# Kernel optimization log

Measured on AMD Instinct MI355X. Metric: run time of the kernel, lower is better.

## Reference

```python
import jax, jax.numpy as jnp
import numpy as np

N_NODES = 10000
N_EDGES = 160000
IN_CH = 512
HID = 512


def setup_inputs() -> dict:
    key = jax.random.key(0)
    k1, k2, k3, k4, k5, k6 = jax.random.split(key, 6)
    x = jax.random.normal(k1, (N_NODES, IN_CH), dtype=jnp.float32)
    # Linear weight, xavier-uniform style scale (torch stores [out, in])
    lim = float(np.sqrt(6.0 / (IN_CH + HID)))
    fc_w = jax.random.uniform(k2, (HID, IN_CH), dtype=jnp.float32, minval=-lim, maxval=lim)
    bias = jnp.zeros((HID,), dtype=jnp.float32)
    prelu_a = jnp.full((1,), 0.25, dtype=jnp.float32)  # torch PReLU default slope
    adj_vals = jax.random.uniform(k3, (N_EDGES,), dtype=jnp.float32)
    adj_row = jnp.sort(jax.random.randint(k4, (N_EDGES,), 0, N_NODES, dtype=jnp.int64))
    adj_col = jax.random.randint(k5, (N_EDGES,), 0, N_NODES, dtype=jnp.int64)
    return {"x": x, "fc_w": fc_w, "bias": bias, "prelu_a": prelu_a,
            "adj_vals": adj_vals, "adj_row": adj_row, "adj_col": adj_col}


def reference(x, fc_w, bias, prelu_a, adj_vals, adj_row, adj_col):
    n_nodes = x.shape[0]
    # x_fts = self.fc(x)  (no bias in fc)
    x_fts = x @ fc_w.T                                   # [N, HID]
    # out = torch.spmm(adj, x_fts): sparse COO matmul via gather + segment_sum
    gathered = adj_vals[:, None] * x_fts[adj_col]        # [E, HID]
    out = jax.ops.segment_sum(gathered, adj_row, num_segments=n_nodes)
    out = out + bias                                     # [N, HID]
    # PReLU with single learned slope
    return jnp.where(out >= 0, out, prelu_a * out)
```

## Files before the change

kernel.cpp:

```cpp
#include <hip/hip_runtime.h>
#include <hip/hip_bf16.h>

typedef __attribute__((ext_vector_type(4))) float f32x4;
typedef __attribute__((ext_vector_type(8))) short bf16x8;

#define NNODES 10000
#define KDIM 512
#define NDIM 512
#define NEDGES 160000
#define RP_BLOCKS 40
#define QV_BLOCKS 157
#define SIDE_BLOCKS (RP_BLOCKS + QV_BLOCKS)
#define GEMM_BLOCKS 628

#define XSCALE 6.0f
#define XQ (127.0f / XSCALE)
#define OUTK (XSCALE / (127.0f * 127.0f))

__device__ __forceinline__ unsigned short f2bf(float f) {
    __hip_bfloat16 h = __float2bfloat16(f);
    return *reinterpret_cast<unsigned short*>(&h);
}

__device__ __forceinline__ bf16x8 cvt8(float4 a, float4 b) {
    bf16x8 r;
    r[0] = (short)f2bf(a.x); r[1] = (short)f2bf(a.y);
    r[2] = (short)f2bf(a.z); r[3] = (short)f2bf(a.w);
    r[4] = (short)f2bf(b.x); r[5] = (short)f2bf(b.y);
    r[6] = (short)f2bf(b.z); r[7] = (short)f2bf(b.w);
    return r;
}

__device__ __forceinline__ int q127(float v, float s) {
    return (int)rintf(fminf(fmaxf(v * s, -127.f), 127.f));
}

#if __has_builtin(__builtin_amdgcn_sdot4)
#define DOT4(a, b, c) __builtin_amdgcn_sdot4((a), (b), (c), false)
#else
__device__ __forceinline__ int dot4_sw(int a, int b, int c) {
    c += (int)(signed char)(a) * (int)(signed char)(b);
    c += (int)(signed char)(a >> 8) * (int)(signed char)(b >> 8);
    c += (int)(signed char)(a >> 16) * (int)(signed char)(b >> 16);
    c += (a >> 24) * (b >> 24);
    return c;
}
#define DOT4(a, b, c) dot4_sw((a), (b), (c))
#endif

__global__ __launch_bounds__(256) void gemm_prep_kernel(
    const float* __restrict__ A, const float* __restrict__ B,
    signed char* __restrict__ X8,
    const int* __restrict__ rows, int* __restrict__ row_ptr,
    const float* __restrict__ vals, int* __restrict__ qvals, int M) {
    __shared__ unsigned short lA[2][64 * 64];
    __shared__ unsigned short lB[2][128 * 64];

    if (blockIdx.x < RP_BLOCKS) {
        int i = blockIdx.x * 256 + threadIdx.x;
        if (i <= NNODES) {
            int lo = 0, hi = NEDGES;
            while (lo < hi) { int mid = (lo + hi) >> 1; if (rows[mid] < i) lo = mid + 1; else hi = mid; }
            row_ptr[i] = lo;
        }
        return;
    }
    if (blockIdx.x < SIDE_BLOCKS) {
        int i = (blockIdx.x - RP_BLOCKS) * 1024 + threadIdx.x * 4;
        if (i < NEDGES) {
            float4 v = *reinterpret_cast<const float4*>(vals + i);
            int4 o;
            o.x = q127(v.x, 127.f); o.y = q127(v.y, 127.f);
            o.z = q127(v.z, 127.f); o.w = q127(v.w, 127.f);
            *reinterpret_cast<int4*>(qvals + i) = o;
        }
        return;
    }

    const int orig = blockIdx.x - SIDE_BLOCKS;
    const int xcd = orig & 7;
    const int base = (xcd < 4) ? xcd * 79 : 4 * 79 + (xcd - 4) * 78;
    const int wgid = base + (orig >> 3);

    const int tid = threadIdx.x;
    const int wid = tid >> 6;
    const int lane = tid & 63;
    const int wc = wid;
    const int m0 = (wgid >> 2) * 64;
    const int n0 = (wgid & 3) * 128;

    const int ar0 = tid >> 3, ar1 = (tid + 256) >> 3;
    const int ag = tid & 7;
    int agr0 = m0 + ar0; if (agr0 >= M) agr0 = M - 1;
    int agr1 = m0 + ar1; if (agr1 >= M) agr1 = M - 1;
    const float* pa0 = A + (size_t)agr0 * KDIM + ag * 8;
    const float* pa1 = A + (size_t)agr1 * KDIM + ag * 8;
    const int wA0 = ar0 * 64 + (ag ^ (ar0 & 7)) * 8;
    const int wA1 = ar1 * 64 + (ag ^ (ar1 & 7)) * 8;
    const int br = tid >> 3;
    const float* pb0 = B + (size_t)(n0 + br) * KDIM + ag * 8;
    const float* pb1 = B + (size_t)(n0 + br + 32) * KDIM + ag * 8;
    const float* pb2 = B + (size_t)(n0 + br + 64) * KDIM + ag * 8;
    const float* pb3 = B + (size_t)(n0 + br + 96) * KDIM + ag * 8;
    const int wB = br * 64 + (ag ^ (br & 7)) * 8;

    f32x4 acc[4][2] = {};
    float4 la0, la1, la2, la3, lb0, lb1, lb2, lb3, lb4, lb5, lb6, lb7;

#define GLOAD(k0)                                                \
    la0 = *reinterpret_cast<const float4*>(pa0 + (k0));          \
    la1 = *reinterpret_cast<const float4*>(pa0 + (k0) + 4);      \
    la2 = *reinterpret_cast<const float4*>(pa1 + (k0));          \
    la3 = *reinterpret_cast<const float4*>(pa1 + (k0) + 4);      \
    lb0 = *reinterpret_cast<const float4*>(pb0 + (k0));          \
    lb1 = *reinterpret_cast<const float4*>(pb0 + (k0) + 4);      \
    lb2 = *reinterpret_cast<const float4*>(pb1 + (k0));          \
    lb3 = *reinterpret_cast<const float4*>(pb1 + (k0) + 4);      \
    lb4 = *reinterpret_cast<const float4*>(pb2 + (k0));          \
    lb5 = *reinterpret_cast<const float4*>(pb2 + (k0) + 4);      \
    lb6 = *reinterpret_cast<const float4*>(pb3 + (k0));          \
    lb7 = *reinterpret_cast<const float4*>(pb3 + (k0) + 4);

#define LWRITE(buf)                                                          \
    *reinterpret_cast<bf16x8*>(lA[buf] + wA0) = cvt8(la0, la1);              \
    *reinterpret_cast<bf16x8*>(lA[buf] + wA1) = cvt8(la2, la3);              \
    *reinterpret_cast<bf16x8*>(lB[buf] + wB) = cvt8(lb0, lb1);               \
    *reinterpret_cast<bf16x8*>(lB[buf] + wB + 32 * 64) = cvt8(lb2, lb3);     \
    *reinterpret_cast<bf16x8*>(lB[buf] + wB + 64 * 64) = cvt8(lb4, lb5);     \
    *reinterpret_cast<bf16x8*>(lB[buf] + wB + 96 * 64) = cvt8(lb6, lb7);

    GLOAD(0)
    LWRITE(0)
    __syncthreads();
    int cur = 0;
#pragma unroll
    for (int kt = 0; kt < 8; kt++) {
        if (kt + 1 < 8) { GLOAD((kt + 1) * 64) }

        bf16x8 af[4][2], bfr[2][2];
#pragma unroll
        for (int i = 0; i < 4; i++)
#pragma unroll
            for (int h = 0; h < 2; h++) {
                int row = i * 16 + (lane & 15);
                int s = (lane >> 4) + h * 4;
                af[i][h] = *reinterpret_cast<const bf16x8*>(
                    lA[cur] + (size_t)row * 64 + (size_t)(s ^ (row & 7)) * 8);
            }
#pragma unroll
        for (int j = 0; j < 2; j++)
#pragma unroll
            for (int h = 0; h < 2; h++) {
                int row = wc * 32 + j * 16 + (lane & 15);
                int s = (lane >> 4) + h * 4;
                bfr[j][h] = *reinterpret_cast<const bf16x8*>(
                    lB[cur] + (size_t)row * 64 + (size_t)(s ^ (row & 7)) * 8);
            }
#pragma unroll
        for (int h = 0; h < 2; h++)
#pragma unroll
            for (int i = 0; i < 4; i++)
#pragma unroll
                for (int j = 0; j < 2; j++)
                    acc[i][j] = __builtin_amdgcn_mfma_f32_16x16x32_bf16(af[i][h], bfr[j][h], acc[i][j], 0, 0, 0);

        if (kt + 1 < 8) { LWRITE(cur ^ 1) }
        __syncthreads();
        cur ^= 1;
    }

#pragma unroll
    for (int i = 0; i < 4; i++) {
#pragma unroll
        for (int r = 0; r < 4; r++) {
            int row = m0 + i * 16 + (lane >> 4) * 4 + r;
            if (row < M) {
#pragma unroll
                for (int j = 0; j < 2; j++) {
                    int col = n0 + wc * 32 + j * 16 + (lane & 15);
                    X8[(size_t)row * NDIM + col] = (signed char)q127(acc[i][j][r], XQ);
                }
            }
        }
    }
}

#define BT4(T0, T1, T2, T3, w0, w1, w2, w3)                          \
    {                                                                \
        unsigned ab_lo = __builtin_amdgcn_perm(w1, w0, 0x05010400u); \
        unsigned ab_hi = __builtin_amdgcn_perm(w1, w0, 0x07030602u); \
        unsigned cd_lo = __builtin_amdgcn_perm(w3, w2, 0x05010400u); \
        unsigned cd_hi = __builtin_amdgcn_perm(w3, w2, 0x07030602u); \
        T0 = __builtin_amdgcn_perm(cd_lo, ab_lo, 0x05040100u);       \
        T1 = __builtin_amdgcn_perm(cd_lo, ab_lo, 0x07060302u);       \
        T2 = __builtin_amdgcn_perm(cd_hi, ab_hi, 0x05040100u);       \
        T3 = __builtin_amdgcn_perm(cd_hi, ab_hi, 0x07060302u);       \
    }

#define EDGE4(ACCV, i)                                                          \
    {                                                                           \
        int4 c4 = *reinterpret_cast<const int4*>(cols + (i));                   \
        int4 q4 = *reinterpret_cast<const int4*>(qvals + (i));                  \
        unsigned qv = (q4.x & 255) | ((q4.y & 255) << 8) |                      \
                      ((q4.z & 255) << 16) | ((unsigned)(q4.w & 255) << 24);    \
        uint2 u0 = *reinterpret_cast<const uint2*>(x8 + (size_t)c4.x * NDIM + lane * 8); \
        uint2 u1 = *reinterpret_cast<const uint2*>(x8 + (size_t)c4.y * NDIM + lane * 8); \
        uint2 u2 = *reinterpret_cast<const uint2*>(x8 + (size_t)c4.z * NDIM + lane * 8); \
        uint2 u3 = *reinterpret_cast<const uint2*>(x8 + (size_t)c4.w * NDIM + lane * 8); \
        unsigned t0, t1, t2, t3, t4, t5, t6, t7;                                \
        BT4(t0, t1, t2, t3, u0.x, u1.x, u2.x, u3.x)                             \
        BT4(t4, t5, t6, t7, u0.y, u1.y, u2.y, u3.y)                             \
        ACCV[0] = DOT4((int)t0, (int)qv, ACCV[0]);                              \
        ACCV[1] = DOT4((int)t1, (int)qv, ACCV[1]);                              \
        ACCV[2] = DOT4((int)t2, (int)qv, ACCV[2]);                              \
        ACCV[3] = DOT4((int)t3, (int)qv, ACCV[3]);                              \
        ACCV[4] = DOT4((int)t4, (int)qv, ACCV[4]);                              \
        ACCV[5] = DOT4((int)t5, (int)qv, ACCV[5]);                              \
        ACCV[6] = DOT4((int)t6, (int)qv, ACCV[6]);                              \
        ACCV[7] = DOT4((int)t7, (int)qv, ACCV[7]);                              \
    }

#define EDGE1(ACCV, i)                                                          \
    {                                                                           \
        int c = cols[i];                                                        \
        int qq = qvals[i];                                                      \
        uint2 u = *reinterpret_cast<const uint2*>(x8 + (size_t)c * NDIM + lane * 8); \
        ACCV[0] += qq * (int)(signed char)(u.x);                                \
        ACCV[1] += qq * (int)(signed char)(u.x >> 8);                           \
        ACCV[2] += qq * (int)(signed char)(u.x >> 16);                          \
        ACCV[3] += qq * ((int)u.x >> 24);                                       \
        ACCV[4] += qq * (int)(signed char)(u.y);                                \
        ACCV[5] += qq * (int)(signed char)(u.y >> 8);                           \
        ACCV[6] += qq * (int)(signed char)(u.y >> 16);                          \
        ACCV[7] += qq * ((int)u.y >> 24);                                       \
    }

__global__ __launch_bounds__(256) void spmm_prelu_kernel(
    const signed char* __restrict__ x8,
    const int* __restrict__ qvals,
    const int* __restrict__ row_ptr,
    const int* __restrict__ cols,
    const float* __restrict__ bias,
    const float* __restrict__ prelu_a,
    float* __restrict__ out) {
    const int lane = threadIdx.x & 63;
    const int gw = (blockIdx.x * 256 + threadIdx.x) >> 6;
    const int nd0 = gw, nd1 = gw + 5000;

    const int s0 = __builtin_amdgcn_readfirstlane(row_ptr[nd0]);
    const int e0 = __builtin_amdgcn_readfirstlane(row_ptr[nd0 + 1]);
    const int s1 = __builtin_amdgcn_readfirstlane(row_ptr[nd1]);
    const int e1 = __builtin_amdgcn_readfirstlane(row_ptr[nd1 + 1]);

    int p[8] = {}, q[8] = {};

    int i0 = s0, i1 = s1;
    while ((i0 + 4 <= e0) && (i1 + 4 <= e1)) {
        EDGE4(p, i0)
        EDGE4(q, i1)
        i0 += 4; i1 += 4;
    }
    for (; i0 + 4 <= e0; i0 += 4) EDGE4(p, i0)
    for (; i0 < e0; i0++) EDGE1(p, i0)
    for (; i1 + 4 <= e1; i1 += 4) EDGE4(q, i1)
    for (; i1 < e1; i1++) EDGE1(q, i1)

    const float4* b4 = reinterpret_cast<const float4*>(bias + lane * 8);
    const float4 bA = b4[0], bB = b4[1];
    const float al = prelu_a[0];

#define EPILOGUE(P, node)                                                        \
    {                                                                            \
        float o0 = (float)P[0] * OUTK + bA.x, o1 = (float)P[1] * OUTK + bA.y;    \
        float o2 = (float)P[2] * OUTK + bA.z, o3 = (float)P[3] * OUTK + bA.w;    \
        float o4 = (float)P[4] * OUTK + bB.x, o5 = (float)P[5] * OUTK + bB.y;    \
        float o6 = (float)P[6] * OUTK + bB.z, o7 = (float)P[7] * OUTK + bB.w;    \
        o0 = (o0 >= 0.f) ? o0 : al * o0;                                         \
        o1 = (o1 >= 0.f) ? o1 : al * o1;                                         \
        o2 = (o2 >= 0.f) ? o2 : al * o2;                                         \
        o3 = (o3 >= 0.f) ? o3 : al * o3;                                         \
        o4 = (o4 >= 0.f) ? o4 : al * o4;                                         \
        o5 = (o5 >= 0.f) ? o5 : al * o5;                                         \
        o6 = (o6 >= 0.f) ? o6 : al * o6;                                         \
        o7 = (o7 >= 0.f) ? o7 : al * o7;                                         \
        f32x4 r0; r0[0] = o0; r0[1] = o1; r0[2] = o2; r0[3] = o3;                \
        f32x4 r1; r1[0] = o4; r1[1] = o5; r1[2] = o6; r1[3] = o7;                \
        f32x4* op = reinterpret_cast<f32x4*>(out + (size_t)(node) * NDIM + lane * 8); \
        __builtin_nontemporal_store(r0, op);                                     \
        __builtin_nontemporal_store(r1, op + 1);                                 \
    }

    EPILOGUE(p, nd0)
    EPILOGUE(q, nd1)
}

extern "C" void kernel_launch(void* const* d_in, const int* in_sizes, int n_in,
                              void* d_out, int out_size, void* d_ws, size_t ws_size,
                              hipStream_t stream) {
    const float* x        = (const float*)d_in[0];
    const float* fc_w     = (const float*)d_in[1];
    const float* bias     = (const float*)d_in[2];
    const float* prelu_a  = (const float*)d_in[3];
    const float* adj_vals = (const float*)d_in[4];
    const int*   adj_row  = (const int*)d_in[5];
    const int*   adj_col  = (const int*)d_in[6];
    float* out = (float*)d_out;

    char* ws = (char*)d_ws;
    signed char* x8 = (signed char*)ws;
    int* row_ptr    = (int*)(ws + 5120000);
    int* qvals      = (int*)(ws + 5160064);

    gemm_prep_kernel<<<SIDE_BLOCKS + GEMM_BLOCKS, 256, 0, stream>>>(
        x, fc_w, x8, adj_row, row_ptr, adj_vals, qvals, NNODES);

    spmm_prelu_kernel<<<1250, 256, 0, stream>>>(x8, qvals, row_ptr, adj_col,
                                                bias, prelu_a, out);
}
```

Baseline: 34.13 us.

## Pre-convert weights to swizzled bf16 and stream them via direct global-to-LDS loads

```diff
diff --git a/kernel.cpp b/kernel.cpp
--- a/kernel.cpp
+++ b/kernel.cpp
@@ -9,8 +9,9 @@
 #define NDIM 512
 #define NEDGES 160000
 #define RP_BLOCKS 40
+#define WB_BLOCKS 128
 #define QV_BLOCKS 157
-#define SIDE_BLOCKS (RP_BLOCKS + QV_BLOCKS)
+#define PREP_BLOCKS (RP_BLOCKS + WB_BLOCKS + QV_BLOCKS)
 #define GEMM_BLOCKS 628
 
 #define XSCALE 6.0f
@@ -48,25 +49,29 @@
 #define DOT4(a, b, c) dot4_sw((a), (b), (c))
 #endif
 
-__global__ __launch_bounds__(256) void gemm_prep_kernel(
-    const float* __restrict__ A, const float* __restrict__ B,
-    signed char* __restrict__ X8,
+__global__ __launch_bounds__(256) void prep_kernel(
+    const float* __restrict__ W, unsigned short* __restrict__ wbs,
     const int* __restrict__ rows, int* __restrict__ row_ptr,
-    const float* __restrict__ vals, int* __restrict__ qvals, int M) {
-    __shared__ unsigned short lA[2][64 * 64];
-    __shared__ unsigned short lB[2][128 * 64];
-
-    if (blockIdx.x < RP_BLOCKS) {
-        int i = blockIdx.x * 256 + threadIdx.x;
+    const float* __restrict__ vals, int* __restrict__ qvals) {
+    const int b = blockIdx.x;
+    if (b < RP_BLOCKS) {
+        int i = b * 256 + threadIdx.x;
         if (i <= NNODES) {
             int lo = 0, hi = NEDGES;
             while (lo < hi) { int mid = (lo + hi) >> 1; if (rows[mid] < i) lo = mid + 1; else hi = mid; }
             row_ptr[i] = lo;
         }
-        return;
-    }
-    if (blockIdx.x < SIDE_BLOCKS) {
-        int i = (blockIdx.x - RP_BLOCKS) * 1024 + threadIdx.x * 4;
+    } else if (b < RP_BLOCKS + WB_BLOCKS) {
+        int idx = ((b - RP_BLOCKS) * 256 + threadIdx.x) * 8;
+        int r = idx >> 9;
+        int c0 = idx & 511;
+        int src = c0 ^ ((r & 7) << 3);
+        const float* pw = W + (size_t)r * KDIM + src;
+        float4 w0 = *reinterpret_cast<const float4*>(pw);
+        float4 w1 = *reinterpret_cast<const float4*>(pw + 4);
+        *reinterpret_cast<bf16x8*>(wbs + (size_t)r * KDIM + c0) = cvt8(w0, w1);
+    } else {
+        int i = (b - RP_BLOCKS - WB_BLOCKS) * 1024 + threadIdx.x * 4;
         if (i < NEDGES) {
             float4 v = *reinterpret_cast<const float4*>(vals + i);
             int4 o;
@@ -74,18 +79,23 @@
             o.z = q127(v.z, 127.f); o.w = q127(v.w, 127.f);
             *reinterpret_cast<int4*>(qvals + i) = o;
         }
-        return;
-    }
-
-    const int orig = blockIdx.x - SIDE_BLOCKS;
+    }
+}
+
+__global__ __launch_bounds__(256) void gemm_kernel(
+    const float* __restrict__ A, const unsigned short* __restrict__ wbs,
+    signed char* __restrict__ X8, int M) {
+    __shared__ unsigned short lA[2][64 * 64];
+    __shared__ unsigned short lB[2][128 * 64];
+
+    const int orig = blockIdx.x;
     const int xcd = orig & 7;
     const int base = (xcd < 4) ? xcd * 79 : 4 * 79 + (xcd - 4) * 78;
     const int wgid = base + (orig >> 3);
 
     const int tid = threadIdx.x;
-    const int wid = tid >> 6;
     const int lane = tid & 63;
-    const int wc = wid;
+    const int wc = tid >> 6;
     const int m0 = (wgid >> 2) * 64;
     const int n0 = (wgid & 3) * 128;
 
@@ -97,45 +107,46 @@
     const float* pa1 = A + (size_t)agr1 * KDIM + ag * 8;
     const int wA0 = ar0 * 64 + (ag ^ (ar0 & 7)) * 8;
     const int wA1 = ar1 * 64 + (ag ^ (ar1 & 7)) * 8;
-    const int br = tid >> 3;
-    const float* pb0 = B + (size_t)(n0 + br) * KDIM + ag * 8;
-    const float* pb1 = B + (size_t)(n0 + br + 32) * KDIM + ag * 8;
-    const float* pb2 = B + (size_t)(n0 + br + 64) * KDIM + ag * 8;
-    const float* pb3 = B + (size_t)(n0 + br + 96) * KDIM + ag * 8;
-    const int wB = br * 64 + (ag ^ (br & 7)) * 8;
+    const int brow = tid >> 3, bpseg = tid & 7;
 
     f32x4 acc[4][2] = {};
-    float4 la0, la1, la2, la3, lb0, lb1, lb2, lb3, lb4, lb5, lb6, lb7;
-
-#define GLOAD(k0)                                                \
+    float4 la0, la1, la2, la3;
+
+#define AGLOAD(k0)                                               \
     la0 = *reinterpret_cast<const float4*>(pa0 + (k0));          \
     la1 = *reinterpret_cast<const float4*>(pa0 + (k0) + 4);      \
     la2 = *reinterpret_cast<const float4*>(pa1 + (k0));          \
-    la3 = *reinterpret_cast<const float4*>(pa1 + (k0) + 4);      \
-    lb0 = *reinterpret_cast<const float4*>(pb0 + (k0));          \
-    lb1 = *reinterpret_cast<const float4*>(pb0 + (k0) + 4);      \
-    lb2 = *reinterpret_cast<const float4*>(pb1 + (k0));          \
-    lb3 = *reinterpret_cast<const float4*>(pb1 + (k0) + 4);      \
-    lb4 = *reinterpret_cast<const float4*>(pb2 + (k0));          \
-    lb5 = *reinterpret_cast<const float4*>(pb2 + (k0) + 4);      \
-    lb6 = *reinterpret_cast<const float4*>(pb3 + (k0));          \
-    lb7 = *reinterpret_cast<const float4*>(pb3 + (k0) + 4);
-
-#define LWRITE(buf)                                                          \
+    la3 = *reinterpret_cast<const float4*>(pa1 + (k0) + 4);
+
+#define ALWRITE(buf)                                                         \
     *reinterpret_cast<bf16x8*>(lA[buf] + wA0) = cvt8(la0, la1);              \
-    *reinterpret_cast<bf16x8*>(lA[buf] + wA1) = cvt8(la2, la3);              \
-    *reinterpret_cast<bf16x8*>(lB[buf] + wB) = cvt8(lb0, lb1);               \
-    *reinterpret_cast<bf16x8*>(lB[buf] + wB + 32 * 64) = cvt8(lb2, lb3);     \
-    *reinterpret_cast<bf16x8*>(lB[buf] + wB + 64 * 64) = cvt8(lb4, lb5);     \
-    *reinterpret_cast<bf16x8*>(lB[buf] + wB + 96 * 64) = cvt8(lb6, lb7);
-
-    GLOAD(0)
-    LWRITE(0)
+    *reinterpret_cast<bf16x8*>(lA[buf] + wA1) = cvt8(la2, la3);
+
+#define BGLOAD(buf, k0)                                                          \
+    {                                                                            \
+        _Pragma("unroll")                                                        \
+        for (int t = 0; t < 4; t++) {                                            \
+            int li = t * 256 + tid;                                              \
+            const unsigned short* gb =                                           \
+                wbs + (size_t)(n0 + brow + t * 32) * KDIM + (k0) + bpseg * 8;    \
+            __builtin_amdgcn_global_load_lds(                                    \
+                (const __attribute__((address_space(1))) void*)gb,               \
+                (__attribute__((address_space(3))) void*)(lB[buf] + (size_t)li * 8), \
+                16, 0, 0);                                                       \
+        }                                                                        \
+    }
+
+    AGLOAD(0)
+    ALWRITE(0)
+    BGLOAD(0, 0)
     __syncthreads();
     int cur = 0;
 #pragma unroll
     for (int kt = 0; kt < 8; kt++) {
-        if (kt + 1 < 8) { GLOAD((kt + 1) * 64) }
+        if (kt + 1 < 8) {
+            BGLOAD(cur ^ 1, (kt + 1) * 64)
+            AGLOAD((kt + 1) * 64)
+        }
 
         bf16x8 af[4][2], bfr[2][2];
 #pragma unroll
@@ -164,7 +175,7 @@
                 for (int j = 0; j < 2; j++)
                     acc[i][j] = __builtin_amdgcn_mfma_f32_16x16x32_bf16(af[i][h], bfr[j][h], acc[i][j], 0, 0, 0);
 
-        if (kt + 1 < 8) { LWRITE(cur ^ 1) }
+        if (kt + 1 < 8) { ALWRITE(cur ^ 1) }
         __syncthreads();
         cur ^= 1;
     }
@@ -228,11 +239,11 @@
         ACCV[0] += qq * (int)(signed char)(u.x);                                \
         ACCV[1] += qq * (int)(signed char)(u.x >> 8);                           \
         ACCV[2] += qq * (int)(signed char)(u.x >> 16);                          \
-        ACCV[3] += qq * ((int)u.x >> 24);                                       \
+        ACCV[3] += qq * ((int)u.x >> 24);                                      \
         ACCV[4] += qq * (int)(signed char)(u.y);                                \
         ACCV[5] += qq * (int)(signed char)(u.y >> 8);                           \
         ACCV[6] += qq * (int)(signed char)(u.y >> 16);                          \
-        ACCV[7] += qq * ((int)u.y >> 24);                                       \
+        ACCV[7] += qq * ((int)u.y >> 24);                                      \
     }
 
 __global__ __launch_bounds__(256) void spmm_prelu_kernel(
@@ -307,12 +318,15 @@
     float* out = (float*)d_out;
 
     char* ws = (char*)d_ws;
-    signed char* x8 = (signed char*)ws;
-    int* row_ptr    = (int*)(ws + 5120000);
-    int* qvals      = (int*)(ws + 5160064);
-
-    gemm_prep_kernel<<<SIDE_BLOCKS + GEMM_BLOCKS, 256, 0, stream>>>(
-        x, fc_w, x8, adj_row, row_ptr, adj_vals, qvals, NNODES);
+    signed char* x8        = (signed char*)ws;
+    int* row_ptr           = (int*)(ws + 5120000);
+    int* qvals             = (int*)(ws + 5160064);
+    unsigned short* wb_swz = (unsigned short*)(ws + 5800080);
+
+    prep_kernel<<<PREP_BLOCKS, 256, 0, stream>>>(fc_w, wb_swz, adj_row, row_ptr,
+                                                 adj_vals, qvals);
+
+    gemm_kernel<<<GEMM_BLOCKS, 256, 0, stream>>>(x, wb_swz, x8, NNODES);
 
     spmm_prelu_kernel<<<1250, 256, 0, stream>>>(x8, qvals, row_ptr, adj_col,
                                                 bias, prelu_a, out);
```

Measured after the change: 39.92 us. 17.0% more time.
